# Optimization experiments

Measured on AMD Instinct MI355X. Metric: run time of the kernel, lower is better.

## Reference

```python
import jax, jax.numpy as jnp
import numpy as np


def _pe_2d(H, W, C, dtype):
    # PositionalEncodingPermute2D: returns (C, H, W)
    ch_half = (C + 1) // 2
    inv = 1.0 / (10000.0 ** (jnp.arange(0, ch_half, 2, dtype=jnp.float32) / ch_half))
    tH = jnp.arange(H, dtype=jnp.float32)
    tW = jnp.arange(W, dtype=jnp.float32)
    sinH = tH[:, None] * inv[None, :]              # (H, ch_half//2)
    sinW = tW[:, None] * inv[None, :]              # (W, ch_half//2)
    embH = jnp.concatenate([jnp.sin(sinH), jnp.cos(sinH)], axis=-1)  # (H, ch_half)
    embW = jnp.concatenate([jnp.sin(sinW), jnp.cos(sinW)], axis=-1)  # (W, ch_half)
    E = jnp.concatenate([
        jnp.broadcast_to(embW[None, :, :], (H, W, ch_half)),
        jnp.broadcast_to(embH[:, None, :], (H, W, ch_half)),
    ], axis=-1)[..., :C]                            # (H, W, C)
    return jnp.transpose(E, (2, 0, 1)).astype(dtype)  # (C, H, W)


def setup_inputs() -> dict:
    key = jax.random.key(0)
    k0, k1, k2, k3 = jax.random.split(key, 4)
    B, C, H, W = 4, 256, 64, 64
    s = 1.0 / np.sqrt(C)  # kaiming-ish scale
    return {
        "x": jax.random.normal(k0, (B, C, H, W), dtype=jnp.float32),
        "wq": jax.random.normal(k1, (C, C), dtype=jnp.float32) * s,
        "wk": jax.random.normal(k2, (C, C), dtype=jnp.float32) * s,
        "wv": jax.random.normal(k3, (C, C), dtype=jnp.float32) * s,
    }


def reference(x, wq, wk, wv):
    B, C, H, W = x.shape
    scale = C ** (-0.5)
    x = x + _pe_2d(H, W, C, x.dtype)[None]          # (B, C, H, W)
    X = x.reshape(B, C, H * W).transpose(0, 2, 1)   # (B, N, C)
    Q = jnp.einsum('bnc,dc->bnd', X, wq)
    K = jnp.einsum('bnc,dc->bnd', X, wk)
    V = jnp.einsum('bnc,dc->bnd', X, wv)
    A = jax.nn.softmax(jnp.einsum('bnd,bmd->bnm', Q, K) * scale, axis=-1)
    Y = jnp.einsum('bnm,bmd->bnd', A, V)            # (B, N, C)
    return Y.transpose(0, 2, 1).reshape(B, C, H, W)
```

## Files before the change

kernel.cpp:

```cpp
#include <hip/hip_runtime.h>
#include <hip/hip_bf16.h>

#define BB 4
#define CC 256
#define NN 4096
#define NSPLIT 4
#define KSPLIT (NN / NSPLIT)
#define NPAIR (KSPLIT / 64)

typedef __attribute__((ext_vector_type(8))) short short8;
typedef __attribute__((ext_vector_type(4))) float floatx4;
typedef __attribute__((ext_vector_type(4))) unsigned short ushortx4;

__device__ __forceinline__ float bf2f(unsigned short u) {
  union { unsigned int i; float f; } cv; cv.i = ((unsigned int)u) << 16; return cv.f;
}
__device__ __forceinline__ unsigned short f2bf(float f) {
  union { __hip_bfloat16 h; unsigned short u; } cv; cv.h = __float2bfloat16(f); return cv.u;
}

#define MFMA(a, b, c) __builtin_amdgcn_mfma_f32_16x16x32_bf16((a), (b), (c), 0, 0, 0)

__device__ __forceinline__ void dma16(const unsigned short* g, unsigned short* l) {
  __builtin_amdgcn_global_load_lds(
      (const __attribute__((address_space(1))) unsigned int*)g,
      (__attribute__((address_space(3))) unsigned int*)l, 16, 0, 0);
}
#define S_BARRIER __builtin_amdgcn_s_barrier()
#define MEMFENCE __asm__ volatile("" ::: "memory")

__global__ __launch_bounds__(256) void wcvt(const float* __restrict__ w0,
                                            const float* __restrict__ w1,
                                            const float* __restrict__ w2,
                                            unsigned short* __restrict__ o0,
                                            unsigned short* __restrict__ o1,
                                            unsigned short* __restrict__ o2) {
  const float* w = (blockIdx.y == 0) ? w0 : (blockIdx.y == 1) ? w1 : w2;
  unsigned short* o = (blockIdx.y == 0) ? o0 : (blockIdx.y == 1) ? o1 : o2;
  int i = (blockIdx.x * 256 + threadIdx.x) * 4;
  floatx4 v = *(const floatx4*)&w[i];
  ushortx4 p;
#pragma unroll
  for (int r = 0; r < 4; r++) p[r] = f2bf(v[r]);
  *(ushortx4*)&o[i] = p;
}

__global__ __launch_bounds__(256) void prep_x(const float* __restrict__ x,
                                              unsigned short* __restrict__ Xbf) {
  __shared__ float tile[32][33];
  int b = blockIdx.z;
  int n0 = blockIdx.x * 32, c0 = blockIdx.y * 32;
  int tx = threadIdx.x, ty = threadIdx.y;
#pragma unroll
  for (int i = 0; i < 4; i++) {
    int c = c0 + ty + i * 8;
    int n = n0 + tx;
    float v = x[((long)(b * CC + c)) * NN + n];
    int hh = n >> 6, ww = n & 63;
    int j = c & 63;
    float freq = exp2f(-0.2076205059304601f * (float)j);
    float arg = (float)((c < 128) ? ww : hh) * freq;
    v += (c & 64) ? cosf(arg) : sinf(arg);
    tile[ty + i * 8][tx] = v;
  }
  __syncthreads();
#pragma unroll
  for (int i = 0; i < 4; i++) {
    int n = n0 + ty + i * 8;
    int c = c0 + tx;
    Xbf[((long)(b * NN + n)) * CC + c] = f2bf(tile[tx][ty + i * 8]);
  }
}

__global__ __launch_bounds__(256, 2) void gemm_fused(const unsigned short* __restrict__ Xbf,
                                                     const unsigned short* __restrict__ Wqk,
                                                     const unsigned short* __restrict__ Wv,
                                                     unsigned short* __restrict__ QK,
                                                     unsigned short* __restrict__ Vt) {
  __shared__ alignas(16) unsigned short Af[2][8 * 512];
  __shared__ alignas(16) unsigned short Bf[2][8 * 512];
  const unsigned short *Ab, *Bb;
  unsigned short* Ob;
  long row0, col0;
  int ldo;
  int F = blockIdx.x;
  if (F < 512) {
    int b = F >> 7, r = F & 127;
    row0 = (long)(r >> 2) * 128;
    col0 = (long)(r & 3) * 128;
    Ab = Xbf + (long)b * NN * CC;
    Bb = Wqk;
    Ob = QK + (long)b * NN * 512;
    ldo = 512;
  } else {
    int F2 = F - 512;
    int b = F2 >> 6, r = F2 & 63;
    row0 = (long)(r >> 5) * 128;
    col0 = (long)(r & 31) * 128;
    Ab = Wv;
    Bb = Xbf + (long)b * NN * CC;
    Ob = Vt + (long)b * CC * NN;
    ldo = NN;
  }
  int t = threadIdx.x, wave = t >> 6, lane = t & 63, quad = lane >> 4, l15 = lane & 15;
  int wr = wave >> 1, wc = wave & 1;

  auto stage = [&](int k0, int buf) {
#pragma unroll
    for (int i = 0; i < 2; i++) {
      int fg = wave * 2 + i;
      dma16(&Ab[(row0 + fg * 16 + l15) * 256 + k0 + quad * 8], &Af[buf][fg * 512]);
      dma16(&Bb[(col0 + fg * 16 + l15) * 256 + k0 + quad * 8], &Bf[buf][fg * 512]);
    }
  };

  floatx4 acc[4][4] = {};
  stage(0, 0);
  MEMFENCE;
#pragma unroll
  for (int ki = 0; ki < 8; ki++) {
    int buf = ki & 1;
    S_BARRIER;
    MEMFENCE;
    if (ki + 1 < 8) {
      stage((ki + 1) * 32, buf ^ 1);
      MEMFENCE;
      __builtin_amdgcn_s_waitcnt(0xF74);
    } else {
      __builtin_amdgcn_s_waitcnt(0xF70);
    }
    S_BARRIER;
    MEMFENCE;
    short8 af[4], bf[4];
#pragma unroll
    for (int i = 0; i < 4; i++) {
      af[i] = *(const short8*)&Af[buf][(wr * 4 + i) * 512 + lane * 8];
      bf[i] = *(const short8*)&Bf[buf][(wc * 4 + i) * 512 + lane * 8];
    }
#pragma unroll
    for (int i = 0; i < 4; i++)
#pragma unroll
      for (int j = 0; j < 4; j++) acc[i][j] = MFMA(af[i], bf[j], acc[i][j]);
  }

#pragma unroll
  for (int i = 0; i < 4; i++)
#pragma unroll
    for (int j = 0; j < 4; j++) {
      long col = col0 + (wc * 4 + j) * 16 + l15;
#pragma unroll
      for (int r = 0; r < 4; r++) {
        long row = row0 + (wr * 4 + i) * 16 + quad * 4 + r;
        Ob[row * (long)ldo + col] = f2bf(acc[i][j][r]);
      }
    }
}

__global__ __launch_bounds__(512, 1) void attn(const unsigned short* __restrict__ QKg,
                                               const unsigned short* __restrict__ Vtg,
                                               unsigned short* __restrict__ Opart,
                                               float* __restrict__ Lp) {
  __shared__ alignas(16) unsigned short Kl[4 * 8192];
  __shared__ alignas(16) unsigned short Vl[4 * 8192];
  __shared__ alignas(16) unsigned short Plf[8][2][512];
  int F = blockIdx.x;
  int c = F & 15, sp = c & 3, b = c >> 2;
  long q0 = (long)(F >> 4) * 256;
  int t = threadIdx.x, wave = t >> 6, lane = t & 63, quad = lane >> 4, l15 = lane & 15;
  const unsigned short* Qb = QKg + (long)b * NN * 512;
  const unsigned short* Kb = Qb + 256;
  const unsigned short* Vb = Vtg + (long)b * CC * NN;

  short8 qf[2][8];
#pragma unroll
  for (int qb = 0; qb < 2; qb++) {
    long qrow = q0 + wave * 32 + qb * 16 + l15;
#pragma unroll
    for (int ks = 0; ks < 8; ks++)
      qf[qb][ks] = *(const short8*)&Qb[qrow * 512 + ks * 32 + quad * 8];
  }

  floatx4 acc[2][17] = {};
  short8 ones;
#pragma unroll
  for (int j = 0; j < 8; j++) ones[j] = (short)0x3F80;

  const float sc = 0.0625f * 1.4426950408889634f;
  const int kbeg = sp * KSPLIT;

  auto stage_pair = [&](int p, int buf) {
#pragma unroll
    for (int tt = 0; tt < 2; tt++) {
      int m0 = kbeg + (p * 2 + tt) * 32;
      int slot = buf * 2 + tt;
#pragma unroll
      for (int st = 0; st < 2; st++) {
        int fg = st * 8 + wave;
        dma16(&Kb[(long)(m0 + st * 16 + l15) * 512 + wave * 32 + quad * 8],
              &Kl[slot * 8192 + fg * 512]);
        dma16(&Vb[(long)(fg * 16 + l15) * NN + m0 + quad * 8],
              &Vl[slot * 8192 + fg * 512]);
      }
    }
  };

  __builtin_amdgcn_s_waitcnt(0xF70);
  stage_pair(0, 0);
  MEMFENCE;

  for (int p = 0; p < NPAIR; p++) {
    int buf = p & 1;
    S_BARRIER;
    MEMFENCE;
    if (p + 1 < NPAIR) {
      stage_pair(p + 1, buf ^ 1);
      MEMFENCE;
      __builtin_amdgcn_s_waitcnt(0xF78);
    } else {
      __builtin_amdgcn_s_waitcnt(0xF70);
    }
    S_BARRIER;
    MEMFENCE;

#pragma unroll
    for (int tt = 0; tt < 2; tt++) {
      int kb = (buf * 2 + tt) * 8192;
      floatx4 s[2][2];
      {
        floatx4 z = {0.f, 0.f, 0.f, 0.f};
        s[0][0] = z; s[0][1] = z; s[1][0] = z; s[1][1] = z;
      }
#pragma unroll
      for (int fgk = 0; fgk < 16; fgk++) {
        short8 kf = *(const short8*)&Kl[kb + fgk * 512 + lane * 8];
        int mt = fgk >> 3, ks = fgk & 7;
        s[0][mt] = MFMA(qf[0][ks], kf, s[0][mt]);
        s[1][mt] = MFMA(qf[1][ks], kf, s[1][mt]);
      }

#pragma unroll
      for (int qb = 0; qb < 2; qb++) {
#pragma unroll
        for (int r = 0; r < 4; r++) {
          unsigned short pb0 = f2bf(__builtin_amdgcn_exp2f(s[qb][0][r] * sc));
          unsigned short pb1 = f2bf(__builtin_amdgcn_exp2f(s[qb][1][r] * sc));
          int m = quad * 4 + r;
          Plf[wave][qb][((l15 >> 3) * 16 + m) * 8 + (l15 & 7)] = pb0;
          Plf[wave][qb][((2 + (l15 >> 3)) * 16 + m) * 8 + (l15 & 7)] = pb1;
        }
      }
      MEMFENCE;
      short8 pf0 = *(const short8*)&Plf[wave][0][lane * 8];
      short8 pf1 = *(const short8*)&Plf[wave][1][lane * 8];
      acc[0][16] = MFMA(pf0, ones, acc[0][16]);
      acc[1][16] = MFMA(pf1, ones, acc[1][16]);
#pragma unroll
      for (int db = 0; db < 16; db++) {
        short8 vf = *(const short8*)&Vl[kb + db * 512 + lane * 8];
        acc[0][db] = MFMA(pf0, vf, acc[0][db]);
        acc[1][db] = MFMA(pf1, vf, acc[1][db]);
      }
      MEMFENCE;
    }
  }

  unsigned short* Ob = Opart + (long)(b * NSPLIT + sp) * CC * NN;
#pragma unroll
  for (int qb = 0; qb < 2; qb++) {
    long nidx = q0 + wave * 32 + qb * 16 + quad * 4;
#pragma unroll
    for (int db = 0; db < 16; db++) {
      long d = db * 16 + l15;
      ushortx4 pk;
#pragma unroll
      for (int r = 0; r < 4; r++) pk[r] = f2bf(acc[qb][db][r]);
      *(ushortx4*)&Ob[d * NN + nidx] = pk;
    }
    if (l15 == 0) {
#pragma unroll
      for (int r = 0; r < 4; r++)
        Lp[(long)(b * NSPLIT + sp) * NN + nidx + r] = acc[qb][16][r];
    }
  }
}

__global__ __launch_bounds__(256) void combine(const unsigned short* __restrict__ Op,
                                               const float* __restrict__ Lp,
                                               float* __restrict__ Out) {
  __shared__ float Wl[64];
  int b = blockIdx.z;
  int d0 = blockIdx.y * 64, n0 = blockIdx.x * 64;
  int t = threadIdx.x;
  if (t < 64) {
    int n = n0 + t;
    float L = 0.f;
#pragma unroll
    for (int s = 0; s < NSPLIT; s++) L += Lp[(long)(b * NSPLIT + s) * NN + n];
    Wl[t] = 1.0f / L;
  }
  __syncthreads();
  int tn = t & 15, td = t >> 4;
  int nb = n0 + tn * 4;
  float w[4];
#pragma unroll
  for (int r = 0; r < 4; r++) w[r] = Wl[tn * 4 + r];
#pragma unroll
  for (int dd = 0; dd < 4; dd++) {
    int d = d0 + td * 4 + dd;
    floatx4 o = {0.f, 0.f, 0.f, 0.f};
#pragma unroll
    for (int s = 0; s < NSPLIT; s++) {
      ushortx4 pv = *(const ushortx4*)&Op[((long)(b * NSPLIT + s) * CC + d) * NN + nb];
#pragma unroll
      for (int r = 0; r < 4; r++) o[r] += bf2f(pv[r]);
    }
#pragma unroll
    for (int r = 0; r < 4; r++) o[r] *= w[r];
    *(floatx4*)&Out[((long)b * CC + d) * NN + nb] = o;
  }
}

extern "C" void kernel_launch(void* const* d_in, const int* in_sizes, int n_in,
                              void* d_out, int out_size, void* d_ws, size_t ws_size,
                              hipStream_t stream) {
  const float* x = (const float*)d_in[0];
  const float* wq = (const float*)d_in[1];
  const float* wk = (const float*)d_in[2];
  const float* wv = (const float*)d_in[3];
  float* out = (float*)d_out;

  char* ws = (char*)d_ws;
  unsigned short* QKbuf = (unsigned short*)(ws);
  unsigned short* Vt = (unsigned short*)(ws + (16l << 20));
  unsigned short* Xbf = (unsigned short*)(ws + (24l << 20));
  unsigned short* Opart = (unsigned short*)(ws + (24l << 20));
  float* Lp = (float*)(ws + (56l << 20));
  unsigned short* Wqk = (unsigned short*)(ws + (57l << 20));
  unsigned short* Wv = (unsigned short*)(ws + (57l << 20) + (1 << 19));

  wcvt<<<dim3(CC * CC / 1024, 3), 256, 0, stream>>>(wq, wk, wv, Wqk, Wqk + CC * CC, Wv);
  prep_x<<<dim3(NN / 32, CC / 32, BB), dim3(32, 8), 0, stream>>>(x, Xbf);
  gemm_fused<<<dim3(768), 256, 0, stream>>>(Xbf, Wqk, Wv, QKbuf, Vt);
  attn<<<dim3(256), 512, 0, stream>>>(QKbuf, Vt, Opart, Lp);
  combine<<<dim3(NN / 64, CC / 64, BB), 256, 0, stream>>>(Opart, Lp, out);
}
```

Measured before the change: 193.1 us.

## Keep softmax probabilities in registers via bpermute and fold scale into Wq

The softmax scale times log2(e) is folded into the bf16 conversion of wq, which removes a per-element multiply before exp2. The QK MFMA operands are swapped so the S tile comes out transposed. The P fragments are then packed with v_cvt_pk_bf16 and rearranged across lanes with ds_bpermute, replacing the LDS store/load round trip. The row sum is accumulated in registers and reduced with shuffles instead of an extra MFMA against a ones vector. It also adds s_setprio around the MFMA loops and raises the launch bound to 2 blocks per CU, which caps VGPRs and risks register spills while the LDS footprint likely still allows only one block.

```diff
diff --git a/kernel.cpp b/kernel.cpp
--- a/kernel.cpp
+++ b/kernel.cpp
@@ -17,6 +17,11 @@
 }
 __device__ __forceinline__ unsigned short f2bf(float f) {
   union { __hip_bfloat16 h; unsigned short u; } cv; cv.h = __float2bfloat16(f); return cv.u;
+}
+__device__ __forceinline__ unsigned int cvtpk_bf16(float lo, float hi) {
+  unsigned int r;
+  asm("v_cvt_pk_bf16_f32 %0, %1, %2" : "=v"(r) : "v"(lo), "v"(hi));
+  return r;
 }
 
 #define MFMA(a, b, c) __builtin_amdgcn_mfma_f32_16x16x32_bf16((a), (b), (c), 0, 0, 0)
@@ -37,11 +42,12 @@
                                             unsigned short* __restrict__ o2) {
   const float* w = (blockIdx.y == 0) ? w0 : (blockIdx.y == 1) ? w1 : w2;
   unsigned short* o = (blockIdx.y == 0) ? o0 : (blockIdx.y == 1) ? o1 : o2;
+  float s = (blockIdx.y == 0) ? 0.0901684400555590f : 1.0f;
   int i = (blockIdx.x * 256 + threadIdx.x) * 4;
   floatx4 v = *(const floatx4*)&w[i];
   ushortx4 p;
 #pragma unroll
-  for (int r = 0; r < 4; r++) p[r] = f2bf(v[r]);
+  for (int r = 0; r < 4; r++) p[r] = f2bf(v[r] * s);
   *(ushortx4*)&o[i] = p;
 }
 
@@ -156,13 +162,12 @@
     }
 }
 
-__global__ __launch_bounds__(512, 1) void attn(const unsigned short* __restrict__ QKg,
+__global__ __launch_bounds__(512, 2) void attn(const unsigned short* __restrict__ QKg,
                                                const unsigned short* __restrict__ Vtg,
                                                unsigned short* __restrict__ Opart,
                                                float* __restrict__ Lp) {
   __shared__ alignas(16) unsigned short Kl[4 * 8192];
   __shared__ alignas(16) unsigned short Vl[4 * 8192];
-  __shared__ alignas(16) unsigned short Plf[8][2][512];
   int F = blockIdx.x;
   int c = F & 15, sp = c & 3, b = c >> 2;
   long q0 = (long)(F >> 4) * 256;
@@ -180,12 +185,13 @@
       qf[qb][ks] = *(const short8*)&Qb[qrow * 512 + ks * 32 + quad * 8];
   }
 
-  floatx4 acc[2][17] = {};
-  short8 ones;
-#pragma unroll
-  for (int j = 0; j < 8; j++) ones[j] = (short)0x3F80;
-
-  const float sc = 0.0625f * 1.4426950408889634f;
+  floatx4 acc[2][16] = {};
+  float rs[2] = {0.f, 0.f};
+
+  const int idx0 = (((lane >> 4) & 1) << 7) | ((lane & 15) << 2);
+  const int idx1 = idx0 + 64;
+  const bool lo32 = lane < 32;
+
   const int kbeg = sp * KSPLIT;
 
   auto stage_pair = [&](int p, int buf) {
@@ -225,42 +231,62 @@
 #pragma unroll
     for (int tt = 0; tt < 2; tt++) {
       int kb = (buf * 2 + tt) * 8192;
-      floatx4 s[2][2];
+      floatx4 s2[2][2];
       {
         floatx4 z = {0.f, 0.f, 0.f, 0.f};
-        s[0][0] = z; s[0][1] = z; s[1][0] = z; s[1][1] = z;
-      }
+        s2[0][0] = z; s2[0][1] = z; s2[1][0] = z; s2[1][1] = z;
+      }
+      __builtin_amdgcn_s_setprio(1);
 #pragma unroll
       for (int fgk = 0; fgk < 16; fgk++) {
         short8 kf = *(const short8*)&Kl[kb + fgk * 512 + lane * 8];
         int mt = fgk >> 3, ks = fgk & 7;
-        s[0][mt] = MFMA(qf[0][ks], kf, s[0][mt]);
-        s[1][mt] = MFMA(qf[1][ks], kf, s[1][mt]);
-      }
-
+        s2[0][mt] = MFMA(kf, qf[0][ks], s2[0][mt]);
+        s2[1][mt] = MFMA(kf, qf[1][ks], s2[1][mt]);
+      }
+      __builtin_amdgcn_s_setprio(0);
+
+      unsigned int pw[2][2][2];
+#pragma unroll
+      for (int qb = 0; qb < 2; qb++)
+#pragma unroll
+        for (int mt = 0; mt < 2; mt++) {
+          float e0 = __builtin_amdgcn_exp2f(s2[qb][mt][0]);
+          float e1 = __builtin_amdgcn_exp2f(s2[qb][mt][1]);
+          float e2 = __builtin_amdgcn_exp2f(s2[qb][mt][2]);
+          float e3 = __builtin_amdgcn_exp2f(s2[qb][mt][3]);
+          rs[qb] += (e0 + e1) + (e2 + e3);
+          pw[qb][mt][0] = cvtpk_bf16(e0, e1);
+          pw[qb][mt][1] = cvtpk_bf16(e2, e3);
+        }
+
+      short8 pf[2];
 #pragma unroll
       for (int qb = 0; qb < 2; qb++) {
-#pragma unroll
-        for (int r = 0; r < 4; r++) {
-          unsigned short pb0 = f2bf(__builtin_amdgcn_exp2f(s[qb][0][r] * sc));
-          unsigned short pb1 = f2bf(__builtin_amdgcn_exp2f(s[qb][1][r] * sc));
-          int m = quad * 4 + r;
-          Plf[wave][qb][((l15 >> 3) * 16 + m) * 8 + (l15 & 7)] = pb0;
-          Plf[wave][qb][((2 + (l15 >> 3)) * 16 + m) * 8 + (l15 & 7)] = pb1;
-        }
-      }
-      MEMFENCE;
-      short8 pf0 = *(const short8*)&Plf[wave][0][lane * 8];
-      short8 pf1 = *(const short8*)&Plf[wave][1][lane * 8];
-      acc[0][16] = MFMA(pf0, ones, acc[0][16]);
-      acc[1][16] = MFMA(pf1, ones, acc[1][16]);
+        unsigned int x0 = (unsigned int)__builtin_amdgcn_ds_bpermute(idx0, (int)pw[qb][0][0]);
+        unsigned int y0 = (unsigned int)__builtin_amdgcn_ds_bpermute(idx0, (int)pw[qb][1][0]);
+        unsigned int x1 = (unsigned int)__builtin_amdgcn_ds_bpermute(idx0, (int)pw[qb][0][1]);
+        unsigned int y1 = (unsigned int)__builtin_amdgcn_ds_bpermute(idx0, (int)pw[qb][1][1]);
+        unsigned int x2 = (unsigned int)__builtin_amdgcn_ds_bpermute(idx1, (int)pw[qb][0][0]);
+        unsigned int y2 = (unsigned int)__builtin_amdgcn_ds_bpermute(idx1, (int)pw[qb][1][0]);
+        unsigned int x3 = (unsigned int)__builtin_amdgcn_ds_bpermute(idx1, (int)pw[qb][0][1]);
+        unsigned int y3 = (unsigned int)__builtin_amdgcn_ds_bpermute(idx1, (int)pw[qb][1][1]);
+        union { unsigned int u[4]; short8 s; } pk;
+        pk.u[0] = lo32 ? x0 : y0;
+        pk.u[1] = lo32 ? x1 : y1;
+        pk.u[2] = lo32 ? x2 : y2;
+        pk.u[3] = lo32 ? x3 : y3;
+        pf[qb] = pk.s;
+      }
+
+      __builtin_amdgcn_s_setprio(1);
 #pragma unroll
       for (int db = 0; db < 16; db++) {
         short8 vf = *(const short8*)&Vl[kb + db * 512 + lane * 8];
-        acc[0][db] = MFMA(pf0, vf, acc[0][db]);
-        acc[1][db] = MFMA(pf1, vf, acc[1][db]);
-      }
-      MEMFENCE;
+        acc[0][db] = MFMA(pf[0], vf, acc[0][db]);
+        acc[1][db] = MFMA(pf[1], vf, acc[1][db]);
+      }
+      __builtin_amdgcn_s_setprio(0);
     }
   }
 
@@ -276,11 +302,11 @@
       for (int r = 0; r < 4; r++) pk[r] = f2bf(acc[qb][db][r]);
       *(ushortx4*)&Ob[d * NN + nidx] = pk;
     }
-    if (l15 == 0) {
-#pragma unroll
-      for (int r = 0; r < 4; r++)
-        Lp[(long)(b * NSPLIT + sp) * NN + nidx + r] = acc[qb][16][r];
-    }
+    float v = rs[qb];
+    v += __shfl_xor(v, 16, 64);
+    v += __shfl_xor(v, 32, 64);
+    if (quad == 0)
+      Lp[(long)(b * NSPLIT + sp) * NN + q0 + wave * 32 + qb * 16 + l15] = v;
   }
 }
 
```

New measurement: 192.8 us. Within noise of the previous version (-0.2%).
